# Kernel optimization log

Hardware: AMD Instinct MI355X
Metric: run time of the kernel (lower is better)

The kernel has to match this reference:

```python
import jax, jax.numpy as jnp
import numpy as np

DIM = 1024
HEADS = 16
DIM_HEAD = 64
INNER = HEADS * DIM_HEAD  # == DIM, so project_out Linear is shape-consistent
SCALE = DIM_HEAD ** -0.5
EPS = 1e-5


def setup_inputs() -> dict:
    key = jax.random.key(0)
    ks = jax.random.split(key, 8)
    std = 0.02
    return {
        "x": jax.random.normal(ks[0], (2, 2048, DIM), dtype=jnp.float32),
        "gamma": jnp.ones((DIM,), dtype=jnp.float32),
        "beta": jnp.zeros((DIM,), dtype=jnp.float32),
        "wq": jax.random.normal(ks[1], (DIM, INNER), dtype=jnp.float32) * std,
        "wk": jax.random.normal(ks[2], (DIM, INNER), dtype=jnp.float32) * std,
        "wv": jax.random.normal(ks[3], (DIM, INNER), dtype=jnp.float32) * std,
        "wo": jax.random.normal(ks[4], (INNER, DIM), dtype=jnp.float32) * std,
        "w_out": jax.random.normal(ks[5], (INNER, DIM), dtype=jnp.float32) * std,
        "b_out": jnp.zeros((DIM,), dtype=jnp.float32),
    }


def reference(x, gamma, beta, wq, wk, wv, wo, w_out, b_out):
    b, n, d = x.shape
    # LayerNorm
    mu = jnp.mean(x, axis=-1, keepdims=True)
    var = jnp.mean(jnp.square(x - mu), axis=-1, keepdims=True)
    xn = (x - mu) * jax.lax.rsqrt(var + EPS) * gamma + beta
    # QKV projections -> [b, h, n, dh]
    def split_heads(t):
        return t.reshape(b, n, HEADS, DIM_HEAD).transpose(0, 2, 1, 3)
    q = split_heads(xn @ wq)
    k = split_heads(xn @ wk)
    v = split_heads(xn @ wv)
    scores = jnp.einsum('bhqd,bhkd->bhqk', q, k) * SCALE
    attn = jax.nn.softmax(scores, axis=-1)
    out = jnp.einsum('bhqk,bhkd->bhqd', attn, v)
    out = out.transpose(0, 2, 1, 3).reshape(b, n, INNER)
    out = out @ wo               # wo: inner -> dim
    out = out @ w_out + b_out    # project_out Linear (dropout=0 -> identity)
    return out
```

## Files before the change

### kernel.cpp

```cpp
#include <hip/hip_runtime.h>

typedef _Float16 f16;
typedef _Float16 f16x2 __attribute__((ext_vector_type(2)));
typedef _Float16 f16x4 __attribute__((ext_vector_type(4)));
typedef _Float16 f16x8 __attribute__((ext_vector_type(8)));
typedef float f32x4 __attribute__((ext_vector_type(4)));

#define MFMA_F16(a, b, c) __builtin_amdgcn_mfma_f32_16x16x32_f16(a, b, c, 0, 0, 0)
#define ASYNC16(g, l) __builtin_amdgcn_global_load_lds(                              \
    (const __attribute__((address_space(1))) void*)(g),                              \
    (__attribute__((address_space(3))) void*)(l), 16, 0, 0)

__global__ __launch_bounds__(256)
void ln_cast_kernel(const float* __restrict__ x, const float* __restrict__ gamma,
                    const float* __restrict__ beta, f16* __restrict__ xn)
{
    const int row = blockIdx.x;
    const float* xr = x + (size_t)row * 1024;
    const int t = threadIdx.x;
    float4 v = *(const float4*)(xr + t * 4);
    float s  = v.x + v.y + v.z + v.w;
    float ss = v.x * v.x + v.y * v.y + v.z * v.z + v.w * v.w;
#pragma unroll
    for (int off = 32; off > 0; off >>= 1) {
        s  += __shfl_down(s, off);
        ss += __shfl_down(ss, off);
    }
    __shared__ float wsum[4], wsq[4];
    const int wid = t >> 6, lane = t & 63;
    if (lane == 0) { wsum[wid] = s; wsq[wid] = ss; }
    __syncthreads();
    const float fs  = wsum[0] + wsum[1] + wsum[2] + wsum[3];
    const float fss = wsq[0] + wsq[1] + wsq[2] + wsq[3];
    const float mu  = fs * (1.0f / 1024.0f);
    const float var = fss * (1.0f / 1024.0f) - mu * mu;
    const float rs  = rsqrtf(var + 1e-5f);
    float4 g = *(const float4*)(gamma + t * 4);
    float4 b = *(const float4*)(beta + t * 4);
    f16x4 o;
    o[0] = (f16)((v.x - mu) * rs * g.x + b.x);
    o[1] = (f16)((v.y - mu) * rs * g.y + b.y);
    o[2] = (f16)((v.z - mu) * rs * g.z + b.z);
    o[3] = (f16)((v.w - mu) * rs * g.w + b.w);
    *(f16x4*)(xn + (size_t)row * 1024 + t * 4) = o;
}

__global__ __launch_bounds__(256)
void prep_w_kernel(const float* __restrict__ wq, const float* __restrict__ wk,
                   const float* __restrict__ wv, const float* __restrict__ wo,
                   const float* __restrict__ wout,
                   f16* __restrict__ wqt, f16* __restrict__ wkt, f16* __restrict__ wvt,
                   f16* __restrict__ wo_h, f16* __restrict__ woutt)
{
    const float* src; f16* dst; int tr; float scl = 1.0f;
    switch (blockIdx.z) {
        case 0:  src = wq;   dst = wqt;   tr = 1; scl = 0.18033688011f; break;
        case 1:  src = wk;   dst = wkt;   tr = 1; break;
        case 2:  src = wv;   dst = wvt;   tr = 1; break;
        case 3:  src = wo;   dst = wo_h;  tr = 0; break;
        default: src = wout; dst = woutt; tr = 1; break;
    }
    const int r0 = blockIdx.y * 64, c0 = blockIdx.x * 64;
    const int t = threadIdx.x;
    if (!tr) {
#pragma unroll
        for (int i = 0; i < 16; i++) {
            int idx = t + 256 * i;
            int r = idx >> 6, c = idx & 63;
            dst[(size_t)(r0 + r) * 1024 + c0 + c] = (f16)src[(size_t)(r0 + r) * 1024 + c0 + c];
        }
    } else {
        __shared__ __align__(16) f16 T[64][72];
#pragma unroll
        for (int i = 0; i < 16; i++) {
            int idx = t + 256 * i;
            int r = idx >> 6, c = idx & 63;
            T[r][c] = (f16)(src[(size_t)(r0 + r) * 1024 + c0 + c] * scl);
        }
        __syncthreads();
#pragma unroll
        for (int i = 0; i < 16; i++) {
            int idx = t + 256 * i;
            int r = idx >> 6, c = idx & 63;
            dst[(size_t)(c0 + r) * 1024 + r0 + c] = T[c][r];
        }
    }
}

template <int EP>
__global__ __launch_bounds__(256, 3)
void gemm_bt(const f16* __restrict__ A, const f16* __restrict__ Bt,
             void* __restrict__ C0, void* __restrict__ C1, void* __restrict__ C2,
             const float* __restrict__ bias, int M, int N, int K)
{
    __shared__ __align__(16) f16 smem[2 * 128 * 64];
    f16* As = smem;
    f16* Bs = smem + 128 * 64;
    const int tid = threadIdx.x;
    const int wid = tid >> 6, lane = tid & 63;
    const int qq = lane >> 4, ml = lane & 15;
    const int row0 = (wid >> 1) * 64, col0 = (wid & 1) * 64;
    const f16* Ab = A + (size_t)blockIdx.x * 128 * K;
    const f16* Bb = Bt + (size_t)blockIdx.y * 128 * K;
    const int sr = lane >> 3;
    const int sc = ((lane & 7) ^ sr) * 8;
    const int swz = ml & 7;

    f32x4 acc[4][4];
#pragma unroll
    for (int i = 0; i < 4; i++)
#pragma unroll
        for (int j = 0; j < 4; j++) acc[i][j] = (f32x4){0.f, 0.f, 0.f, 0.f};

    for (int k0 = 0; k0 < K; k0 += 64) {
        __syncthreads();
#pragma unroll
        for (int j = 0; j < 4; j++) {
            const int inst = wid * 4 + j;
            const int r = inst * 8 + sr;
            ASYNC16(Ab + (size_t)r * K + k0 + sc, &As[inst * 512]);
            ASYNC16(Bb + (size_t)r * K + k0 + sc, &Bs[inst * 512]);
        }
        __syncthreads();
#pragma unroll
        for (int kh = 0; kh < 2; kh++) {
            f16x8 af[4], bf[4];
#pragma unroll
            for (int mb = 0; mb < 4; mb++)
                af[mb] = *(const f16x8*)(&As[(row0 + mb * 16 + ml) * 64 + ((kh * 4 + qq) ^ swz) * 8]);
#pragma unroll
            for (int nb = 0; nb < 4; nb++)
                bf[nb] = *(const f16x8*)(&Bs[(col0 + nb * 16 + ml) * 64 + ((kh * 4 + qq) ^ swz) * 8]);
#pragma unroll
            for (int mb = 0; mb < 4; mb++)
#pragma unroll
                for (int nb = 0; nb < 4; nb++)
                    acc[mb][nb] = MFMA_F16(af[mb], bf[nb], acc[mb][nb]);
        }
    }

    const int rT = blockIdx.x * 128 + row0 + qq * 4;
    if (EP == 3) {
        float* C = (float*)C0;
#pragma unroll
        for (int mb = 0; mb < 4; mb++)
#pragma unroll
            for (int nb = 0; nb < 4; nb++) {
                int c = blockIdx.y * 128 + col0 + nb * 16 + ml;
                float bv = bias[c];
#pragma unroll
                for (int rg = 0; rg < 4; rg++)
                    C[(size_t)(rT + mb * 16 + rg) * N + c] = acc[mb][nb][rg] + bv;
            }
    } else if (EP == 2) {
        f16* C = (f16*)C0;
#pragma unroll
        for (int mb = 0; mb < 4; mb++)
#pragma unroll
            for (int nb = 0; nb < 4; nb++) {
                int c = blockIdx.y * 128 + col0 + nb * 16 + ml;
#pragma unroll
                for (int rg = 0; rg < 4; rg++)
                    C[(size_t)(rT + mb * 16 + rg) * N + c] = (f16)acc[mb][nb][rg];
            }
    } else {
        __syncthreads();
        f16* Cs = smem;
        const int sel = (blockIdx.y * 128) >> 10;
        const int bb  = (blockIdx.x * 128) >> 11;
        const int nl0 = (blockIdx.x * 128) & 2047;
        const int h0  = (blockIdx.y & 7) * 2;
        if (sel < 2) {
#pragma unroll
            for (int mb = 0; mb < 4; mb++)
#pragma unroll
                for (int nb = 0; nb < 4; nb++) {
                    int col = col0 + nb * 16 + ml;
#pragma unroll
                    for (int rg = 0; rg < 4; rg++) {
                        int row = row0 + mb * 16 + qq * 4 + rg;
                        int ch = (col >> 3) ^ (row & 15);
                        Cs[row * 128 + ch * 8 + (col & 7)] = (f16)acc[mb][nb][rg];
                    }
                }
            __syncthreads();
            f16* Dst = (f16*)(sel == 0 ? C0 : C1);
#pragma unroll
            for (int i = 0; i < 8; i++) {
                int idx = i * 256 + tid;
                int r = idx >> 4, ch = idx & 15;
                f16x8 v = *(const f16x8*)(&Cs[r * 128 + ((ch ^ (r & 15)) * 8)]);
                int hh = h0 + (ch >> 3), d0 = (ch & 7) * 8;
                *(f16x8*)(Dst + ((size_t)(bb * 16 + hh) * 2048 + nl0 + r) * 64 + d0) = v;
            }
        } else {
#pragma unroll
            for (int mb = 0; mb < 4; mb++)
#pragma unroll
                for (int nb = 0; nb < 4; nb++) {
                    int col = col0 + nb * 16 + ml;
                    int rch = ((row0 + mb * 16) >> 3) + (qq >> 1);
                    int ch = rch ^ (col & 15);
                    f16x4 w;
                    w[0] = (f16)acc[mb][nb][0]; w[1] = (f16)acc[mb][nb][1];
                    w[2] = (f16)acc[mb][nb][2]; w[3] = (f16)acc[mb][nb][3];
                    *(f16x4*)(&Cs[col * 128 + ch * 8 + (qq & 1) * 4]) = w;
                }
            __syncthreads();
            f16* Dst = (f16*)C2;
#pragma unroll
            for (int i = 0; i < 8; i++) {
                int idx = i * 256 + tid;
                int c = idx >> 4, tc = idx & 15;
                f16x8 v = *(const f16x8*)(&Cs[c * 128 + ((tc ^ (c & 15)) * 8)]);
                int hh = h0 + (c >> 6), d = c & 63;
                *(f16x8*)(Dst + ((size_t)(bb * 16 + hh) * 64 + d) * 2048 + nl0 + tc * 8) = v;
            }
        }
    }
}

__global__ __launch_bounds__(256, 2)
void flash_kernel(const f16* __restrict__ Q, const f16* __restrict__ K,
                  const f16* __restrict__ Vt, f16* __restrict__ O)
{
    __shared__ __align__(16) f16 Ks[128 * 64];
    __shared__ __align__(16) f16 Vts[64 * 128];
    __shared__ __align__(16) f16 Ps[4][32 * 128];

    const int bh = blockIdx.y;
    const int q0 = blockIdx.x * 128;
    const int tid = threadIdx.x, wid = tid >> 6, lane = tid & 63;
    const int qq = lane >> 4, ml = lane & 15;

    const f16* Qb = Q + ((size_t)bh * 2048 + q0 + wid * 32) * 64;
    const f16* Kb = K + (size_t)bh * 2048 * 64;
    const f16* Vb = Vt + (size_t)bh * 64 * 2048;

    f16x8 qf[2][2];
#pragma unroll
    for (int mb = 0; mb < 2; mb++)
#pragma unroll
        for (int kh = 0; kh < 2; kh++)
            qf[mb][kh] = *(const f16x8*)(Qb + (size_t)(mb * 16 + ml) * 64 + kh * 32 + qq * 8);

    f32x4 oacc[2][4];
    float lsum[2] = {0.f, 0.f};
#pragma unroll
    for (int mb = 0; mb < 2; mb++)
#pragma unroll
        for (int nd = 0; nd < 4; nd++) oacc[mb][nd] = (f32x4){0.f, 0.f, 0.f, 0.f};

    const int sr = lane >> 3, sc8 = ((lane & 7) ^ sr) * 8;
    const int rv = lane >> 4, cv = lane & 15;
    f16* Psw = Ps[wid];

    for (int t0 = 0; t0 < 2048; t0 += 128) {
        __syncthreads();
#pragma unroll
        for (int j = 0; j < 4; j++) {
            const int inst = wid * 4 + j;
            const int kr = inst * 8 + sr;
            ASYNC16(Kb + ((size_t)t0 + kr) * 64 + sc8, &Ks[inst * 512]);
            const int vr = inst * 4 + rv;
            ASYNC16(Vb + (size_t)vr * 2048 + t0 + ((cv ^ (vr & 15)) * 8), &Vts[inst * 512]);
        }
        __syncthreads();

        f32x4 s[2][8];
#pragma unroll
        for (int mb = 0; mb < 2; mb++)
#pragma unroll
            for (int nb = 0; nb < 8; nb++) s[mb][nb] = (f32x4){0.f, 0.f, 0.f, 0.f};
#pragma unroll
        for (int nb = 0; nb < 8; nb++)
#pragma unroll
            for (int kh = 0; kh < 2; kh++) {
                f16x8 kb = *(const f16x8*)(&Ks[(nb * 16 + ml) * 64 + ((kh * 4 + qq) ^ (ml & 7)) * 8]);
                s[0][nb] = MFMA_F16(kb, qf[0][kh], s[0][nb]);
                s[1][nb] = MFMA_F16(kb, qf[1][kh], s[1][nb]);
            }

#pragma unroll
        for (int mb = 0; mb < 2; mb++)
#pragma unroll
            for (int nb = 0; nb < 8; nb++) {
                float p0 = __builtin_amdgcn_exp2f(s[mb][nb][0]);
                float p1 = __builtin_amdgcn_exp2f(s[mb][nb][1]);
                float p2 = __builtin_amdgcn_exp2f(s[mb][nb][2]);
                float p3 = __builtin_amdgcn_exp2f(s[mb][nb][3]);
                lsum[mb] += (p0 + p1) + (p2 + p3);
                f16x2 lo = __builtin_bit_cast(f16x2, __builtin_amdgcn_cvt_pkrtz(p0, p1));
                f16x2 hi = __builtin_bit_cast(f16x2, __builtin_amdgcn_cvt_pkrtz(p2, p3));
                f16x4 w; w[0] = lo[0]; w[1] = lo[1]; w[2] = hi[0]; w[3] = hi[1];
                int ch = (2 * nb + (qq >> 1)) ^ ml;
                *(f16x4*)(&Psw[(mb * 16 + ml) * 128 + ch * 8 + (qq & 1) * 4]) = w;
            }

#pragma unroll
        for (int ks = 0; ks < 4; ks++) {
            const int rc = ((ks * 4 + qq) ^ ml) * 8;
            f16x8 pa0 = *(const f16x8*)(&Psw[ml * 128 + rc]);
            f16x8 pa1 = *(const f16x8*)(&Psw[(16 + ml) * 128 + rc]);
#pragma unroll
            for (int nd = 0; nd < 4; nd++) {
                f16x8 vb = *(const f16x8*)(&Vts[(nd * 16 + ml) * 128 + rc]);
                oacc[0][nd] = MFMA_F16(pa0, vb, oacc[0][nd]);
                oacc[1][nd] = MFMA_F16(pa1, vb, oacc[1][nd]);
            }
        }
    }

#pragma unroll
    for (int mb = 0; mb < 2; mb++) {
        lsum[mb] += __shfl_xor(lsum[mb], 16);
        lsum[mb] += __shfl_xor(lsum[mb], 32);
    }

    const int bb = bh >> 4, hh = bh & 15;
#pragma unroll
    for (int mb = 0; mb < 2; mb++)
#pragma unroll
        for (int r = 0; r < 4; r++) {
            float linv = 1.0f / __shfl(lsum[mb], qq * 4 + r, 16);
            int tok = q0 + wid * 32 + mb * 16 + qq * 4 + r;
            size_t base = ((size_t)(bb * 2048 + tok)) * 1024 + hh * 64;
#pragma unroll
            for (int nd = 0; nd < 4; nd++)
                O[base + nd * 16 + ml] = (f16)(oacc[mb][nd][r] * linv);
        }
}

extern "C" void kernel_launch(void* const* d_in, const int* in_sizes, int n_in,
                              void* d_out, int out_size, void* d_ws, size_t ws_size,
                              hipStream_t stream)
{
    const float* x     = (const float*)d_in[0];
    const float* gamma = (const float*)d_in[1];
    const float* beta  = (const float*)d_in[2];
    const float* wq    = (const float*)d_in[3];
    const float* wk    = (const float*)d_in[4];
    const float* wv    = (const float*)d_in[5];
    const float* wo    = (const float*)d_in[6];
    const float* wout  = (const float*)d_in[7];
    const float* bout  = (const float*)d_in[8];
    float* out = (float*)d_out;

    char* ws = (char*)d_ws;
    const size_t MB = 1 << 20;
    f16* xn    = (f16*)(ws + 0);
    f16* wqt   = (f16*)(ws + 8 * MB);
    f16* wkt   = (f16*)(ws + 10 * MB);
    f16* wvt   = (f16*)(ws + 12 * MB);
    f16* wo_h  = (f16*)(ws + 14 * MB);
    f16* woutt = (f16*)(ws + 16 * MB);
    f16* W2t   = (f16*)(ws + 18 * MB);
    f16* Qh    = (f16*)(ws + 20 * MB);
    f16* Kh    = (f16*)(ws + 28 * MB);
    f16* Vth   = (f16*)(ws + 36 * MB);
    f16* Oh    = xn;

    ln_cast_kernel<<<4096, 256, 0, stream>>>(x, gamma, beta, xn);
    prep_w_kernel<<<dim3(16, 16, 5), 256, 0, stream>>>(wq, wk, wv, wo, wout,
                                                       wqt, wkt, wvt, wo_h, woutt);
    gemm_bt<0><<<dim3(32, 24), 256, 0, stream>>>(xn, wqt, Qh, Kh, Vth, nullptr, 4096, 3072, 1024);
    gemm_bt<2><<<dim3(8, 8), 256, 0, stream>>>(woutt, wo_h, W2t, nullptr, nullptr, nullptr, 1024, 1024, 1024);
    flash_kernel<<<dim3(16, 32), 256, 0, stream>>>(Qh, Kh, Vth, Oh);
    gemm_bt<3><<<dim3(32, 8), 256, 0, stream>>>(Oh, W2t, out, nullptr, nullptr, bout, 4096, 1024, 1024);
}
```

Measured before the change: 209.6 us.

## Merge prep launches and load flash K/V fragments directly from global memory

```diff
diff --git a/kernel.cpp b/kernel.cpp
--- a/kernel.cpp
+++ b/kernel.cpp
@@ -12,56 +12,57 @@
     (__attribute__((address_space(3))) void*)(l), 16, 0, 0)
 
 __global__ __launch_bounds__(256)
-void ln_cast_kernel(const float* __restrict__ x, const float* __restrict__ gamma,
-                    const float* __restrict__ beta, f16* __restrict__ xn)
+void pre_kernel(const float* __restrict__ x, const float* __restrict__ gamma,
+                const float* __restrict__ beta, f16* __restrict__ xn,
+                const float* __restrict__ wq, const float* __restrict__ wk,
+                const float* __restrict__ wv, const float* __restrict__ wo,
+                const float* __restrict__ wout,
+                f16* __restrict__ wqt, f16* __restrict__ wkt, f16* __restrict__ wvt,
+                f16* __restrict__ wo_h, f16* __restrict__ woutt)
 {
-    const int row = blockIdx.x;
-    const float* xr = x + (size_t)row * 1024;
     const int t = threadIdx.x;
-    float4 v = *(const float4*)(xr + t * 4);
-    float s  = v.x + v.y + v.z + v.w;
-    float ss = v.x * v.x + v.y * v.y + v.z * v.z + v.w * v.w;
-#pragma unroll
-    for (int off = 32; off > 0; off >>= 1) {
-        s  += __shfl_down(s, off);
-        ss += __shfl_down(ss, off);
-    }
-    __shared__ float wsum[4], wsq[4];
-    const int wid = t >> 6, lane = t & 63;
-    if (lane == 0) { wsum[wid] = s; wsq[wid] = ss; }
-    __syncthreads();
-    const float fs  = wsum[0] + wsum[1] + wsum[2] + wsum[3];
-    const float fss = wsq[0] + wsq[1] + wsq[2] + wsq[3];
-    const float mu  = fs * (1.0f / 1024.0f);
-    const float var = fss * (1.0f / 1024.0f) - mu * mu;
-    const float rs  = rsqrtf(var + 1e-5f);
-    float4 g = *(const float4*)(gamma + t * 4);
-    float4 b = *(const float4*)(beta + t * 4);
-    f16x4 o;
-    o[0] = (f16)((v.x - mu) * rs * g.x + b.x);
-    o[1] = (f16)((v.y - mu) * rs * g.y + b.y);
-    o[2] = (f16)((v.z - mu) * rs * g.z + b.z);
-    o[3] = (f16)((v.w - mu) * rs * g.w + b.w);
-    *(f16x4*)(xn + (size_t)row * 1024 + t * 4) = o;
-}
-
-__global__ __launch_bounds__(256)
-void prep_w_kernel(const float* __restrict__ wq, const float* __restrict__ wk,
-                   const float* __restrict__ wv, const float* __restrict__ wo,
-                   const float* __restrict__ wout,
-                   f16* __restrict__ wqt, f16* __restrict__ wkt, f16* __restrict__ wvt,
-                   f16* __restrict__ wo_h, f16* __restrict__ woutt)
-{
+    if (blockIdx.x < 4096) {
+        const int row = blockIdx.x;
+        const float* xr = x + (size_t)row * 1024;
+        float4 v = *(const float4*)(xr + t * 4);
+        float s  = v.x + v.y + v.z + v.w;
+        float ss = v.x * v.x + v.y * v.y + v.z * v.z + v.w * v.w;
+#pragma unroll
+        for (int off = 32; off > 0; off >>= 1) {
+            s  += __shfl_down(s, off);
+            ss += __shfl_down(ss, off);
+        }
+        __shared__ float wsum[4], wsq[4];
+        const int wid = t >> 6, lane = t & 63;
+        if (lane == 0) { wsum[wid] = s; wsq[wid] = ss; }
+        __syncthreads();
+        const float fs  = wsum[0] + wsum[1] + wsum[2] + wsum[3];
+        const float fss = wsq[0] + wsq[1] + wsq[2] + wsq[3];
+        const float mu  = fs * (1.0f / 1024.0f);
+        const float var = fss * (1.0f / 1024.0f) - mu * mu;
+        const float rs  = rsqrtf(var + 1e-5f);
+        float4 g = *(const float4*)(gamma + t * 4);
+        float4 b = *(const float4*)(beta + t * 4);
+        f16x4 o;
+        o[0] = (f16)((v.x - mu) * rs * g.x + b.x);
+        o[1] = (f16)((v.y - mu) * rs * g.y + b.y);
+        o[2] = (f16)((v.z - mu) * rs * g.z + b.z);
+        o[3] = (f16)((v.w - mu) * rs * g.w + b.w);
+        *(f16x4*)(xn + (size_t)row * 1024 + t * 4) = o;
+        return;
+    }
+    const int pb = blockIdx.x - 4096;
+    const int z = pb >> 8, rem = pb & 255;
+    const int bx = rem & 15, by = rem >> 4;
     const float* src; f16* dst; int tr; float scl = 1.0f;
-    switch (blockIdx.z) {
+    switch (z) {
         case 0:  src = wq;   dst = wqt;   tr = 1; scl = 0.18033688011f; break;
         case 1:  src = wk;   dst = wkt;   tr = 1; break;
         case 2:  src = wv;   dst = wvt;   tr = 1; break;
         case 3:  src = wo;   dst = wo_h;  tr = 0; break;
         default: src = wout; dst = woutt; tr = 1; break;
     }
-    const int r0 = blockIdx.y * 64, c0 = blockIdx.x * 64;
-    const int t = threadIdx.x;
+    const int r0 = by * 64, c0 = bx * 64;
     if (!tr) {
 #pragma unroll
         for (int i = 0; i < 16; i++) {
@@ -87,11 +88,11 @@
     }
 }
 
-template <int EP>
 __global__ __launch_bounds__(256, 3)
-void gemm_bt(const f16* __restrict__ A, const f16* __restrict__ Bt,
-             void* __restrict__ C0, void* __restrict__ C1, void* __restrict__ C2,
-             const float* __restrict__ bias, int M, int N, int K)
+void gemm_qkv_w2(const f16* __restrict__ A, const f16* __restrict__ Bt,
+                 f16* __restrict__ Qd, f16* __restrict__ Kd, f16* __restrict__ Vd,
+                 const f16* __restrict__ A2, const f16* __restrict__ Bt2,
+                 f16* __restrict__ W2t)
 {
     __shared__ __align__(16) f16 smem[2 * 128 * 64];
     f16* As = smem;
@@ -100,8 +101,18 @@
     const int wid = tid >> 6, lane = tid & 63;
     const int qq = lane >> 4, ml = lane & 15;
     const int row0 = (wid >> 1) * 64, col0 = (wid & 1) * 64;
-    const f16* Ab = A + (size_t)blockIdx.x * 128 * K;
-    const f16* Bb = Bt + (size_t)blockIdx.y * 128 * K;
+
+    int mode, bx, by;
+    const f16 *Abase, *Bbase;
+    if (blockIdx.y < 24) {
+        mode = 0; bx = blockIdx.x; by = blockIdx.y; Abase = A; Bbase = Bt;
+    } else {
+        mode = 1;
+        int id = (blockIdx.y - 24) * 32 + blockIdx.x;
+        bx = id & 7; by = id >> 3; Abase = A2; Bbase = Bt2;
+    }
+    const f16* Ab = Abase + (size_t)bx * 128 * 1024;
+    const f16* Bb = Bbase + (size_t)by * 128 * 1024;
     const int sr = lane >> 3;
     const int sc = ((lane & 7) ^ sr) * 8;
     const int swz = ml & 7;
@@ -112,14 +123,14 @@
 #pragma unroll
         for (int j = 0; j < 4; j++) acc[i][j] = (f32x4){0.f, 0.f, 0.f, 0.f};
 
-    for (int k0 = 0; k0 < K; k0 += 64) {
+    for (int k0 = 0; k0 < 1024; k0 += 64) {
         __syncthreads();
 #pragma unroll
         for (int j = 0; j < 4; j++) {
             const int inst = wid * 4 + j;
             const int r = inst * 8 + sr;
-            ASYNC16(Ab + (size_t)r * K + k0 + sc, &As[inst * 512]);
-            ASYNC16(Bb + (size_t)r * K + k0 + sc, &Bs[inst * 512]);
+            ASYNC16(Ab + (size_t)r * 1024 + k0 + sc, &As[inst * 512]);
+            ASYNC16(Bb + (size_t)r * 1024 + k0 + sc, &Bs[inst * 512]);
         }
         __syncthreads();
 #pragma unroll
@@ -139,83 +150,69 @@
         }
     }
 
-    const int rT = blockIdx.x * 128 + row0 + qq * 4;
-    if (EP == 3) {
-        float* C = (float*)C0;
+    if (mode == 1) {
+        const int rT = bx * 128 + row0 + qq * 4;
 #pragma unroll
         for (int mb = 0; mb < 4; mb++)
 #pragma unroll
             for (int nb = 0; nb < 4; nb++) {
-                int c = blockIdx.y * 128 + col0 + nb * 16 + ml;
-                float bv = bias[c];
+                int c = by * 128 + col0 + nb * 16 + ml;
 #pragma unroll
                 for (int rg = 0; rg < 4; rg++)
-                    C[(size_t)(rT + mb * 16 + rg) * N + c] = acc[mb][nb][rg] + bv;
-            }
-    } else if (EP == 2) {
-        f16* C = (f16*)C0;
+                    W2t[(size_t)(rT + mb * 16 + rg) * 1024 + c] = (f16)acc[mb][nb][rg];
+            }
+        return;
+    }
+    __syncthreads();
+    f16* Cs = smem;
+    const int sel = (by * 128) >> 10;
+    const int bb  = (bx * 128) >> 11;
+    const int nl0 = (bx * 128) & 2047;
+    const int h0  = (by & 7) * 2;
+    if (sel < 2) {
 #pragma unroll
         for (int mb = 0; mb < 4; mb++)
 #pragma unroll
             for (int nb = 0; nb < 4; nb++) {
-                int c = blockIdx.y * 128 + col0 + nb * 16 + ml;
-#pragma unroll
-                for (int rg = 0; rg < 4; rg++)
-                    C[(size_t)(rT + mb * 16 + rg) * N + c] = (f16)acc[mb][nb][rg];
-            }
+                int col = col0 + nb * 16 + ml;
+#pragma unroll
+                for (int rg = 0; rg < 4; rg++) {
+                    int row = row0 + mb * 16 + qq * 4 + rg;
+                    int ch = (col >> 3) ^ (row & 15);
+                    Cs[row * 128 + ch * 8 + (col & 7)] = (f16)acc[mb][nb][rg];
+                }
+            }
+        __syncthreads();
+        f16* Dst = (sel == 0 ? Qd : Kd);
+#pragma unroll
+        for (int i = 0; i < 8; i++) {
+            int idx = i * 256 + tid;
+            int r = idx >> 4, ch = idx & 15;
+            f16x8 v = *(const f16x8*)(&Cs[r * 128 + ((ch ^ (r & 15)) * 8)]);
+            int hh = h0 + (ch >> 3), d0 = (ch & 7) * 8;
+            *(f16x8*)(Dst + ((size_t)(bb * 16 + hh) * 2048 + nl0 + r) * 64 + d0) = v;
+        }
     } else {
-        __syncthreads();
-        f16* Cs = smem;
-        const int sel = (blockIdx.y * 128) >> 10;
-        const int bb  = (blockIdx.x * 128) >> 11;
-        const int nl0 = (blockIdx.x * 128) & 2047;
-        const int h0  = (blockIdx.y & 7) * 2;
-        if (sel < 2) {
-#pragma unroll
-            for (int mb = 0; mb < 4; mb++)
-#pragma unroll
-                for (int nb = 0; nb < 4; nb++) {
-                    int col = col0 + nb * 16 + ml;
-#pragma unroll
-                    for (int rg = 0; rg < 4; rg++) {
-                        int row = row0 + mb * 16 + qq * 4 + rg;
-                        int ch = (col >> 3) ^ (row & 15);
-                        Cs[row * 128 + ch * 8 + (col & 7)] = (f16)acc[mb][nb][rg];
-                    }
-                }
-            __syncthreads();
-            f16* Dst = (f16*)(sel == 0 ? C0 : C1);
-#pragma unroll
-            for (int i = 0; i < 8; i++) {
-                int idx = i * 256 + tid;
-                int r = idx >> 4, ch = idx & 15;
-                f16x8 v = *(const f16x8*)(&Cs[r * 128 + ((ch ^ (r & 15)) * 8)]);
-                int hh = h0 + (ch >> 3), d0 = (ch & 7) * 8;
-                *(f16x8*)(Dst + ((size_t)(bb * 16 + hh) * 2048 + nl0 + r) * 64 + d0) = v;
-            }
-        } else {
-#pragma unroll
-            for (int mb = 0; mb < 4; mb++)
-#pragma unroll
-                for (int nb = 0; nb < 4; nb++) {
-                    int col = col0 + nb * 16 + ml;
-                    int rch = ((row0 + mb * 16) >> 3) + (qq >> 1);
-                    int ch = rch ^ (col & 15);
-                    f16x4 w;
-                    w[0] = (f16)acc[mb][nb][0]; w[1] = (f16)acc[mb][nb][1];
-                    w[2] = (f16)acc[mb][nb][2]; w[3] = (f16)acc[mb][nb][3];
-                    *(f16x4*)(&Cs[col * 128 + ch * 8 + (qq & 1) * 4]) = w;
-                }
-            __syncthreads();
-            f16* Dst = (f16*)C2;
-#pragma unroll
-            for (int i = 0; i < 8; i++) {
-                int idx = i * 256 + tid;
-                int c = idx >> 4, tc = idx & 15;
-                f16x8 v = *(const f16x8*)(&Cs[c * 128 + ((tc ^ (c & 15)) * 8)]);
-                int hh = h0 + (c >> 6), d = c & 63;
-                *(f16x8*)(Dst + ((size_t)(bb * 16 + hh) * 64 + d) * 2048 + nl0 + tc * 8) = v;
-            }
+#pragma unroll
+        for (int mb = 0; mb < 4; mb++)
+#pragma unroll
+            for (int nb = 0; nb < 4; nb++) {
+                int col = col0 + nb * 16 + ml;
+                int rch = ((row0 + mb * 16) >> 3) + (qq >> 1);
+                int ch = rch ^ (col & 15);
+                f16x4 w;
+                w[0] = (f16)acc[mb][nb][0]; w[1] = (f16)acc[mb][nb][1];
+                w[2] = (f16)acc[mb][nb][2]; w[3] = (f16)acc[mb][nb][3];
+                *(f16x4*)(&Cs[col * 128 + ch * 8 + (qq & 1) * 4]) = w;
+            }
+        __syncthreads();
+#pragma unroll
+        for (int i = 0; i < 8; i++) {
+            int idx = i * 256 + tid;
+            int c = idx >> 4, tc = idx & 15;
+            f16x8 v = *(const f16x8*)(&Cs[c * 128 + ((tc ^ (c & 15)) * 8)]);
+            int hh = h0 + (c >> 6), d = c & 63;
+            *(f16x8*)(Vd + ((size_t)(bb * 16 + hh) * 64 + d) * 2048 + nl0 + tc * 8) = v;
         }
     }
 }
@@ -224,8 +221,6 @@
 void flash_kernel(const f16* __restrict__ Q, const f16* __restrict__ K,
                   const f16* __restrict__ Vt, f16* __restrict__ O)
 {
-    __shared__ __align__(16) f16 Ks[128 * 64];
-    __shared__ __align__(16) f16 Vts[64 * 128];
     __shared__ __align__(16) f16 Ps[4][32 * 128];
 
     const int bh = blockIdx.y;
@@ -234,8 +229,8 @@
     const int qq = lane >> 4, ml = lane & 15;
 
     const f16* Qb = Q + ((size_t)bh * 2048 + q0 + wid * 32) * 64;
-    const f16* Kb = K + (size_t)bh * 2048 * 64;
-    const f16* Vb = Vt + (size_t)bh * 64 * 2048;
+    const f16* Kb = K + (size_t)bh * 2048 * 64 + (size_t)ml * 64 + qq * 8;
+    const f16* Vb = Vt + (size_t)bh * 64 * 2048 + (size_t)ml * 2048 + qq * 8;
 
     f16x8 qf[2][2];
 #pragma unroll
@@ -251,21 +246,15 @@
 #pragma unroll
         for (int nd = 0; nd < 4; nd++) oacc[mb][nd] = (f32x4){0.f, 0.f, 0.f, 0.f};
 
-    const int sr = lane >> 3, sc8 = ((lane & 7) ^ sr) * 8;
-    const int rv = lane >> 4, cv = lane & 15;
     f16* Psw = Ps[wid];
 
     for (int t0 = 0; t0 < 2048; t0 += 128) {
-        __syncthreads();
-#pragma unroll
-        for (int j = 0; j < 4; j++) {
-            const int inst = wid * 4 + j;
-            const int kr = inst * 8 + sr;
-            ASYNC16(Kb + ((size_t)t0 + kr) * 64 + sc8, &Ks[inst * 512]);
-            const int vr = inst * 4 + rv;
-            ASYNC16(Vb + (size_t)vr * 2048 + t0 + ((cv ^ (vr & 15)) * 8), &Vts[inst * 512]);
-        }
-        __syncthreads();
+        f16x8 kf[8][2];
+#pragma unroll
+        for (int nb = 0; nb < 8; nb++)
+#pragma unroll
+            for (int kh = 0; kh < 2; kh++)
+                kf[nb][kh] = *(const f16x8*)(Kb + (size_t)(t0 + nb * 16) * 64 + kh * 32);
 
         f32x4 s[2][8];
 #pragma unroll
@@ -276,10 +265,16 @@
         for (int nb = 0; nb < 8; nb++)
 #pragma unroll
             for (int kh = 0; kh < 2; kh++) {
-                f16x8 kb = *(const f16x8*)(&Ks[(nb * 16 + ml) * 64 + ((kh * 4 + qq) ^ (ml & 7)) * 8]);
-                s[0][nb] = MFMA_F16(kb, qf[0][kh], s[0][nb]);
-                s[1][nb] = MFMA_F16(kb, qf[1][kh], s[1][nb]);
-            }
+                s[0][nb] = MFMA_F16(kf[nb][kh], qf[0][kh], s[0][nb]);
+                s[1][nb] = MFMA_F16(kf[nb][kh], qf[1][kh], s[1][nb]);
+            }
+
+        f16x8 vf[4][4];
+#pragma unroll
+        for (int ks = 0; ks < 4; ks++)
+#pragma unroll
+            for (int nd = 0; nd < 4; nd++)
+                vf[ks][nd] = *(const f16x8*)(Vb + (size_t)(nd * 16) * 2048 + t0 + ks * 32);
 
 #pragma unroll
         for (int mb = 0; mb < 2; mb++)
@@ -292,7 +287,7 @@
                 lsum[mb] += (p0 + p1) + (p2 + p3);
                 f16x2 lo = __builtin_bit_cast(f16x2, __builtin_amdgcn_cvt_pkrtz(p0, p1));
                 f16x2 hi = __builtin_bit_cast(f16x2, __builtin_amdgcn_cvt_pkrtz(p2, p3));
-                f16x4 w; w[0] = lo[0]; w[1] = lo[1]; w[2] = hi[0]; w[3] = hi[1];
+                f16x4 w = __builtin_shufflevector(lo, hi, 0, 1, 2, 3);
                 int ch = (2 * nb + (qq >> 1)) ^ ml;
                 *(f16x4*)(&Psw[(mb * 16 + ml) * 128 + ch * 8 + (qq & 1) * 4]) = w;
             }
@@ -304,9 +299,8 @@
             f16x8 pa1 = *(const f16x8*)(&Psw[(16 + ml) * 128 + rc]);
 #pragma unroll
             for (int nd = 0; nd < 4; nd++) {
-                f16x8 vb = *(const f16x8*)(&Vts[(nd * 16 + ml) * 128 + rc]);
-                oacc[0][nd] = MFMA_F16(pa0, vb, oacc[0][nd]);
-                oacc[1][nd] = MFMA_F16(pa1, vb, oacc[1][nd]);
+                oacc[0][nd] = MFMA_F16(pa0, vf[ks][nd], oacc[0][nd]);
+                oacc[1][nd] = MFMA_F16(pa1, vf[ks][nd], oacc[1][nd]);
             }
         }
     }
@@ -328,6 +322,69 @@
 #pragma unroll
             for (int nd = 0; nd < 4; nd++)
                 O[base + nd * 16 + ml] = (f16)(oacc[mb][nd][r] * linv);
+        }
+}
+
+__global__ __launch_bounds__(256, 3)
+void gemm_final(const f16* __restrict__ A, const f16* __restrict__ Bt,
+                float* __restrict__ C, const float* __restrict__ bias)
+{
+    __shared__ __align__(16) f16 smem[2 * 128 * 64];
+    f16* As = smem;
+    f16* Bs = smem + 128 * 64;
+    const int tid = threadIdx.x;
+    const int wid = tid >> 6, lane = tid & 63;
+    const int qq = lane >> 4, ml = lane & 15;
+    const int row0 = (wid >> 1) * 64, col0 = (wid & 1) * 64;
+    const f16* Ab = A + (size_t)blockIdx.x * 128 * 1024;
+    const f16* Bb = Bt + (size_t)blockIdx.y * 128 * 1024;
+    const int sr = lane >> 3;
+    const int sc = ((lane & 7) ^ sr) * 8;
+    const int swz = ml & 7;
+
+    f32x4 acc[4][4];
+#pragma unroll
+    for (int i = 0; i < 4; i++)
+#pragma unroll
+        for (int j = 0; j < 4; j++) acc[i][j] = (f32x4){0.f, 0.f, 0.f, 0.f};
+
+    for (int k0 = 0; k0 < 1024; k0 += 64) {
+        __syncthreads();
+#pragma unroll
+        for (int j = 0; j < 4; j++) {
+            const int inst = wid * 4 + j;
+            const int r = inst * 8 + sr;
+            ASYNC16(Ab + (size_t)r * 1024 + k0 + sc, &As[inst * 512]);
+            ASYNC16(Bb + (size_t)r * 1024 + k0 + sc, &Bs[inst * 512]);
+        }
+        __syncthreads();
+#pragma unroll
+        for (int kh = 0; kh < 2; kh++) {
+            f16x8 af[4], bf[4];
+#pragma unroll
+            for (int mb = 0; mb < 4; mb++)
+                af[mb] = *(const f16x8*)(&As[(row0 + mb * 16 + ml) * 64 + ((kh * 4 + qq) ^ swz) * 8]);
+#pragma unroll
+            for (int nb = 0; nb < 4; nb++)
+                bf[nb] = *(const f16x8*)(&Bs[(col0 + nb * 16 + ml) * 64 + ((kh * 4 + qq) ^ swz) * 8]);
+#pragma unroll
+            for (int mb = 0; mb < 4; mb++)
+#pragma unroll
+                for (int nb = 0; nb < 4; nb++)
+                    acc[mb][nb] = MFMA_F16(af[mb], bf[nb], acc[mb][nb]);
+        }
+    }
+
+    const int rT = blockIdx.x * 128 + row0 + qq * 4;
+#pragma unroll
+    for (int mb = 0; mb < 4; mb++)
+#pragma unroll
+        for (int nb = 0; nb < 4; nb++) {
+            int c = blockIdx.y * 128 + col0 + nb * 16 + ml;
+            float bv = bias[c];
+#pragma unroll
+            for (int rg = 0; rg < 4; rg++)
+                C[(size_t)(rT + mb * 16 + rg) * 1024 + c] = acc[mb][nb][rg] + bv;
         }
 }
 
@@ -360,11 +417,10 @@
     f16* Vth   = (f16*)(ws + 36 * MB);
     f16* Oh    = xn;
 
-    ln_cast_kernel<<<4096, 256, 0, stream>>>(x, gamma, beta, xn);
-    prep_w_kernel<<<dim3(16, 16, 5), 256, 0, stream>>>(wq, wk, wv, wo, wout,
-                                                       wqt, wkt, wvt, wo_h, woutt);
-    gemm_bt<0><<<dim3(32, 24), 256, 0, stream>>>(xn, wqt, Qh, Kh, Vth, nullptr, 4096, 3072, 1024);
-    gemm_bt<2><<<dim3(8, 8), 256, 0, stream>>>(woutt, wo_h, W2t, nullptr, nullptr, nullptr, 1024, 1024, 1024);
+    pre_kernel<<<5376, 256, 0, stream>>>(x, gamma, beta, xn, wq, wk, wv, wo, wout,
+                                         wqt, wkt, wvt, wo_h, woutt);
+    gemm_qkv_w2<<<dim3(32, 26), 256, 0, stream>>>(xn, wqt, Qh, Kh, Vth,
+                                                  woutt, wo_h, W2t);
     flash_kernel<<<dim3(16, 32), 256, 0, stream>>>(Qh, Kh, Vth, Oh);
-    gemm_bt<3><<<dim3(32, 8), 256, 0, stream>>>(Oh, W2t, out, nullptr, nullptr, bout, 4096, 1024, 1024);
+    gemm_final<<<dim3(32, 8), 256, 0, stream>>>(Oh, W2t, out, bout);
 }
```

New measurement: 269.3 us. +28.5%, slower.
